# Optimization experiments

Hardware: AMD Instinct MI355X
Metric: run time of the kernel (lower is better)

Reference implementation:

```python
import jax, jax.numpy as jnp
import numpy as np

B, C, D, H, W = 2, 64, 12, 256, 64


def _conv1x1_relu(x, w, b):
    # x: (B, C, D, H, W); w: (C_out, C_in); b: (C_out,)
    y = jnp.einsum('oc,bcdhw->bodhw', w, x) + b[None, :, None, None, None]
    return jax.nn.relu(y)


def setup_inputs() -> dict:
    key = jax.random.key(0)
    ks = jax.random.split(key, 9)
    s = 1.0 / np.sqrt(C)
    inp = {
        'rep': jax.random.normal(ks[0], (B, C, D, H, W), dtype=jnp.float32),
        'Wq_w': jax.random.normal(ks[1], (C, C), dtype=jnp.float32) * s,
        'Wq_b': jnp.zeros((C,), dtype=jnp.float32),
        'Wk_w': jax.random.normal(ks[2], (C, C), dtype=jnp.float32) * s,
        'Wk_b': jnp.zeros((C,), dtype=jnp.float32),
        'Wv_w': jax.random.normal(ks[3], (C, C), dtype=jnp.float32) * s,
        'Wv_b': jnp.zeros((C,), dtype=jnp.float32),
        'FC_w': jax.random.normal(ks[4], (C, C), dtype=jnp.float32) * s,
        'FC_b': jnp.zeros((C,), dtype=jnp.float32),
    }
    return inp


def reference(rep, Wq_w, Wq_b, Wk_w, Wk_b, Wv_w, Wv_b, FC_w, FC_b):
    # 1x1x1 conv projections + ReLU, then permute to (B, D, W, H, C)
    q = _conv1x1_relu(rep, Wq_w, Wq_b).transpose(0, 2, 4, 3, 1)
    k = _conv1x1_relu(rep, Wk_w, Wk_b).transpose(0, 2, 4, 3, 1)
    v = _conv1x1_relu(rep, Wv_w, Wv_b).transpose(0, 2, 4, 3, 1)
    # attention over H axis: scores (B, D, W, H, H)
    scores = jnp.einsum('bdwhc,bdwgc->bdwhg', q, k) / jnp.sqrt(jnp.asarray(C, rep.dtype))
    attn = jax.nn.softmax(scores, axis=-1)
    out = jnp.einsum('bdwhg,bdwgc->bdwhc', attn, v)
    # permute(0,4,1,3,2): (B, D, W, H, C) -> (B, C, D, H, W)
    out = out.transpose(0, 4, 1, 3, 2)
    return _conv1x1_relu(out, FC_w, FC_b)
```

## Files before the change

### kernel.cpp

```cpp
#include <hip/hip_runtime.h>

typedef float f32x4 __attribute__((ext_vector_type(4)));
typedef short bf16x8 __attribute__((ext_vector_type(8)));
typedef unsigned short ushort_t;

#define NB 2
#define NC 64
#define ND 12
#define NH 256
#define NW 64
#define CSTRIDE (ND*NH*NW)
#define QSZ_ELEMS (24*64*256*64)
#define WS_NEED   ((size_t)3*QSZ_ELEMS*2)

__device__ __forceinline__ ushort_t bf_round(float f){
    unsigned int u = __float_as_uint(f);
    return (ushort_t)((u + 0x7fffu + ((u >> 16) & 1u)) >> 16);
}
__device__ __forceinline__ float bf_to_f(ushort_t s){ return __uint_as_float(((unsigned int)s) << 16); }

union U4S8 { uint4 u; bf16x8 s; };

__device__ __forceinline__ int row64_off(int r, int o){
    return r*128 + ((((o>>3) ^ (r&7)))<<4) + (o&7)*2;
}
__device__ __forceinline__ int row64_chunk(int r, int kchunk){
    return r*128 + (((kchunk ^ (r&7)))<<4);
}
__device__ __forceinline__ int vt_off(int c, int g){
    return c*512 + ((((g>>3) ^ (c&7)))<<4) + (g&7)*2;
}
__device__ __forceinline__ int vt_chunk(int c, int gchunk){
    return c*512 + (((gchunk ^ (c&7)))<<4);
}

__device__ __forceinline__ U4S8 wfrag_f(const float* W, int hl, int G, int ot, int m){
    const float* p2 = W + (hl + 16*ot)*NC + 32*m + 8*G;
    float4 f0 = *(const float4*)p2;
    float4 f1 = *(const float4*)(p2 + 4);
    U4S8 u; ushort_t* s = (ushort_t*)&u;
    s[0]=bf_round(f0.x); s[1]=bf_round(f0.y); s[2]=bf_round(f0.z); s[3]=bf_round(f0.w);
    s[4]=bf_round(f1.x); s[5]=bf_round(f1.y); s[6]=bf_round(f1.z); s[7]=bf_round(f1.w);
    return u;
}

__global__ __launch_bounds__(256, 2) void k1_proj(
    const float* __restrict__ rep,
    const float* __restrict__ Wq, const float* __restrict__ bq,
    const float* __restrict__ Wk, const float* __restrict__ bk,
    const float* __restrict__ Wv, const float* __restrict__ bv,
    ushort_t* __restrict__ qws, ushort_t* __restrict__ kws, ushort_t* __restrict__ vws)
{
    __shared__ __align__(16) unsigned char smem[65536];
    unsigned char* XL = smem;
    unsigned char* OB = smem + 32768;

    const int t = threadIdx.x, lane = t & 63, wid = t >> 6;
    const int G = lane >> 4, hl = lane & 15;
    const int blk = blockIdx.x;
    const int bd = blk >> 6;
    const int h0 = (blk & 63) * 4;
    const int d = bd % ND, b = bd / ND;
    const long dbase2 = (long)b*NC*CSTRIDE + (long)d*(NH*NW) + (long)h0*NW;

#pragma unroll
    for (int oct = 0; oct < 8; ++oct){
        float f[8];
#pragma unroll
        for (int j = 0; j < 8; ++j)
            f[j] = rep[dbase2 + (long)(8*oct + j)*CSTRIDE + t];
        U4S8 u; ushort_t* s = (ushort_t*)&u;
#pragma unroll
        for (int j = 0; j < 8; ++j) s[j] = bf_round(f[j]);
        *(uint4*)(XL + row64_chunk(t, oct)) = u.u;
    }
    __syncthreads();

    U4S8 xa[4][2];
#pragma unroll
    for (int nt = 0; nt < 4; ++nt)
#pragma unroll
        for (int m = 0; m < 2; ++m)
            xa[nt][m].u = *(const uint4*)(XL + row64_chunk(64*wid + 16*nt + hl, 4*m + G));

    auto pass = [&](const float* W, const float* bias, float scale, ushort_t* dst){
        U4S8 bw[4][2];
        float bb[4];
#pragma unroll
        for (int ot = 0; ot < 4; ++ot){
            bw[ot][0] = wfrag_f(W, hl, G, ot, 0);
            bw[ot][1] = wfrag_f(W, hl, G, ot, 1);
            bb[ot] = bias[hl + 16*ot];
        }
        f32x4 acc[4][4];
#pragma unroll
        for (int nt = 0; nt < 4; ++nt)
#pragma unroll
            for (int ot = 0; ot < 4; ++ot){
                f32x4 a = {0.f,0.f,0.f,0.f};
                a = __builtin_amdgcn_mfma_f32_16x16x32_bf16(xa[nt][0].s, bw[ot][0].s, a, 0,0,0);
                a = __builtin_amdgcn_mfma_f32_16x16x32_bf16(xa[nt][1].s, bw[ot][1].s, a, 0,0,0);
#pragma unroll
                for (int r = 0; r < 4; ++r) a[r] = fmaxf(a[r] + bb[ot], 0.f) * scale;
                acc[nt][ot] = a;
            }
#pragma unroll
        for (int nt = 0; nt < 4; ++nt)
#pragma unroll
            for (int ot = 0; ot < 4; ++ot)
#pragma unroll
                for (int r = 0; r < 4; ++r){
                    int n = 64*wid + 16*nt + 4*G + r;
                    int o = hl + 16*ot;
                    *(ushort_t*)(OB + row64_off(n, o)) = bf_round(acc[nt][ot][r]);
                }
        __syncthreads();
#pragma unroll
        for (int i = 0; i < 8; ++i){
            int g2 = i*256 + t; int n = g2 >> 3; int c8 = g2 & 7;
            uint4 u = *(const uint4*)(OB + row64_chunk(n, c8));
            long row_g = ((long)bd*64 + (n & 63))*256 + h0 + (n >> 6);
            *(uint4*)((unsigned char*)dst + row_g*128 + c8*16) = u;
        }
        __syncthreads();
    };
    pass(Wq, bq, 0.125f, qws);
    pass(Wk, bk, 1.0f,   kws);
    pass(Wv, bv, 1.0f,   vws);
}

__global__ __launch_bounds__(256, 2) void k2_attn(
    ushort_t* __restrict__ qws, const ushort_t* __restrict__ kws, const ushort_t* __restrict__ vws)
{
    __shared__ __align__(16) unsigned char smem[65536];
    unsigned char* KL = smem;
    unsigned char* VT = smem + 32768;

    const int t = threadIdx.x, lane = t & 63, wid = t >> 6;
    const int G = lane >> 4, hl = lane & 15;
    const int bdw = blockIdx.x;
    ushort_t* qslice = qws + (size_t)bdw*16384;
    const unsigned char* kslice = (const unsigned char*)(kws + (size_t)bdw*16384);
    const unsigned char* vslice = (const unsigned char*)(vws + (size_t)bdw*16384);

#pragma unroll
    for (int i = 0; i < 8; ++i){
        int g2 = i*256 + t; int g = g2 >> 3; int c8 = g2 & 7;
        uint4 ku = *(const uint4*)(kslice + g2*16);
        *(uint4*)(KL + row64_chunk(g, c8)) = ku;
        U4S8 vu; vu.u = *(const uint4*)(vslice + g2*16);
#pragma unroll
        for (int j = 0; j < 8; ++j)
            *(ushort_t*)(VT + vt_off(8*c8 + j, g)) = (ushort_t)vu.s[j];
    }
    __syncthreads();

    U4S8 qfr[4][2];
#pragma unroll
    for (int ht = 0; ht < 4; ++ht)
#pragma unroll
        for (int m = 0; m < 2; ++m)
            qfr[ht][m].u = *(const uint4*)((const unsigned char*)qslice
                              + (64*wid + 16*ht + hl)*128 + (4*m + G)*16);

    f32x4 oacc[4][4];
#pragma unroll
    for (int ct = 0; ct < 4; ++ct)
#pragma unroll
        for (int ht = 0; ht < 4; ++ht) oacc[ct][ht] = (f32x4){0.f,0.f,0.f,0.f};
    float m_run[4], l_run[4];
#pragma unroll
    for (int ht = 0; ht < 4; ++ht){ m_run[ht] = -1e30f; l_run[ht] = 0.f; }

    const int srcq0 = (16*((2*G    ) & 3) + hl)*4;
    const int srcq1 = (16*((2*G + 1) & 3) + hl)*4;

    for (int gb = 0; gb < NH; gb += 64){
        U4S8 kfr[4][2];
#pragma unroll
        for (int gt = 0; gt < 4; ++gt)
#pragma unroll
            for (int m = 0; m < 2; ++m)
                kfr[gt][m].u = *(const uint4*)(KL + row64_chunk(gb + 16*gt + hl, 4*m + G));

        f32x4 sacc[4][4];
#pragma unroll
        for (int gt = 0; gt < 4; ++gt)
#pragma unroll
            for (int ht = 0; ht < 4; ++ht){
                f32x4 a = {0.f,0.f,0.f,0.f};
                a = __builtin_amdgcn_mfma_f32_16x16x32_bf16(kfr[gt][0].s, qfr[ht][0].s, a, 0,0,0);
                a = __builtin_amdgcn_mfma_f32_16x16x32_bf16(kfr[gt][1].s, qfr[ht][1].s, a, 0,0,0);
                sacc[gt][ht] = a;
            }

        unsigned int pk[4][4][2];
#pragma unroll
        for (int ht = 0; ht < 4; ++ht){
            float cm = -1e30f;
#pragma unroll
            for (int gt = 0; gt < 4; ++gt)
#pragma unroll
                for (int r = 0; r < 4; ++r) cm = fmaxf(cm, sacc[gt][ht][r]);
            cm = fmaxf(cm, __shfl_xor(cm, 16));
            cm = fmaxf(cm, __shfl_xor(cm, 32));
            const float mn  = fmaxf(m_run[ht], cm);
            const float corr = __expf(m_run[ht] - mn);
            m_run[ht] = mn;
            float ls = 0.f;
#pragma unroll
            for (int gt = 0; gt < 4; ++gt){
                f32x4 s = sacc[gt][ht];
                float e0 = __expf(s[0]-mn), e1 = __expf(s[1]-mn);
                float e2 = __expf(s[2]-mn), e3 = __expf(s[3]-mn);
                ls += (e0+e1)+(e2+e3);
                pk[ht][gt][0] = (unsigned int)bf_round(e0) | ((unsigned int)bf_round(e1) << 16);
                pk[ht][gt][1] = (unsigned int)bf_round(e2) | ((unsigned int)bf_round(e3) << 16);
            }
            ls += __shfl_xor(ls, 16);
            ls += __shfl_xor(ls, 32);
            l_run[ht] = l_run[ht]*corr + ls;
#pragma unroll
            for (int ct = 0; ct < 4; ++ct)
#pragma unroll
                for (int r = 0; r < 4; ++r) oacc[ct][ht][r] *= corr;
        }

        U4S8 vfr[4][2];
#pragma unroll
        for (int ct = 0; ct < 4; ++ct)
#pragma unroll
            for (int m = 0; m < 2; ++m)
                vfr[ct][m].u = *(const uint4*)(VT + vt_chunk(16*ct + hl, (gb>>3) + 4*m + G));

#pragma unroll
        for (int m = 0; m < 2; ++m){
            U4S8 bfr[4];
#pragma unroll
            for (int ht = 0; ht < 4; ++ht){
                unsigned int wv[4];
#pragma unroll
                for (int jj = 0; jj < 4; ++jj){
                    const int src = (jj >> 1) ? srcq1 : srcq0;
                    const int p2  = jj & 1;
                    int rA = __builtin_amdgcn_ds_bpermute(src, (int)pk[ht][2*m  ][p2]);
                    int rB = __builtin_amdgcn_ds_bpermute(src, (int)pk[ht][2*m+1][p2]);
                    wv[jj] = (lane < 32) ? (unsigned int)rA : (unsigned int)rB;
                }
                bfr[ht].u = make_uint4(wv[0], wv[1], wv[2], wv[3]);
            }
#pragma unroll
            for (int ct = 0; ct < 4; ++ct)
#pragma unroll
                for (int ht = 0; ht < 4; ++ht)
                    oacc[ct][ht] = __builtin_amdgcn_mfma_f32_16x16x32_bf16(vfr[ct][m].s, bfr[ht].s, oacc[ct][ht], 0,0,0);
        }
    }

    float invl[4];
#pragma unroll
    for (int ht = 0; ht < 4; ++ht) invl[ht] = 1.f / l_run[ht];

    __syncthreads();
#pragma unroll
    for (int ct = 0; ct < 4; ++ct)
#pragma unroll
        for (int ht = 0; ht < 4; ++ht)
#pragma unroll
            for (int r = 0; r < 4; ++r){
                int h = 64*wid + 16*ht + hl;
                int c = 16*ct + 4*G + r;
                *(ushort_t*)(KL + row64_off(h, c)) = bf_round(oacc[ct][ht][r] * invl[ht]);
            }
    __syncthreads();
#pragma unroll
    for (int i = 0; i < 8; ++i){
        int g2 = i*256 + t;
        uint4 u = *(const uint4*)(KL + row64_chunk(g2 >> 3, g2 & 7));
        *(uint4*)((unsigned char*)qslice + g2*16) = u;
    }
}

__global__ __launch_bounds__(256, 2) void k3_fc(
    const ushort_t* __restrict__ ows, const float* __restrict__ Wf, const float* __restrict__ bfc,
    float* __restrict__ out)
{
    __shared__ __align__(16) float YL[16384];

    const int t = threadIdx.x, lane = t & 63, wid = t >> 6;
    const int G = lane >> 4, hl = lane & 15;
    const int blk = blockIdx.x;
    const int bd = blk >> 6;
    const int h0 = (blk & 63) * 4;
    const int d = bd % ND, b = bd / ND;

    U4S8 xa[4][2];
#pragma unroll
    for (int nt = 0; nt < 4; ++nt)
#pragma unroll
        for (int m = 0; m < 2; ++m){
            long row_g = ((long)bd*64 + (16*nt + hl))*256 + h0 + wid;
            xa[nt][m].u = *(const uint4*)((const unsigned char*)ows + row_g*128 + (4*m + G)*16);
        }

    U4S8 bw[4][2];
    float bb[4];
#pragma unroll
    for (int ot = 0; ot < 4; ++ot){
        bw[ot][0] = wfrag_f(Wf, hl, G, ot, 0);
        bw[ot][1] = wfrag_f(Wf, hl, G, ot, 1);
        bb[ot] = bfc[hl + 16*ot];
    }

    f32x4 acc[4][4];
#pragma unroll
    for (int nt = 0; nt < 4; ++nt)
#pragma unroll
        for (int ot = 0; ot < 4; ++ot){
            f32x4 a = {0.f,0.f,0.f,0.f};
            a = __builtin_amdgcn_mfma_f32_16x16x32_bf16(xa[nt][0].s, bw[ot][0].s, a, 0,0,0);
            a = __builtin_amdgcn_mfma_f32_16x16x32_bf16(xa[nt][1].s, bw[ot][1].s, a, 0,0,0);
#pragma unroll
            for (int r = 0; r < 4; ++r) a[r] = fmaxf(a[r] + bb[ot], 0.f);
            acc[nt][ot] = a;
        }

#pragma unroll
    for (int nt = 0; nt < 4; ++nt)
#pragma unroll
        for (int ot = 0; ot < 4; ++ot)
#pragma unroll
            for (int r = 0; r < 4; ++r){
                int n = 64*wid + 16*nt + 4*G + r;
                int o = hl + 16*ot;
                YL[(n<<6) + (o ^ ((n>>2)&31))] = acc[nt][ot][r];
            }
    __syncthreads();

    const long base3 = (long)b*NC*CSTRIDE + (long)d*(NH*NW) + (long)h0*NW;
#pragma unroll
    for (int i = 0; i < 16; ++i){
        int idx = i*1024 + t*4;
        int o = idx >> 8;
        int n0 = idx & 255;
        int osw = o ^ (t & 31);
        float4 v;
        v.x = YL[((n0+0)<<6) + osw];
        v.y = YL[((n0+1)<<6) + osw];
        v.z = YL[((n0+2)<<6) + osw];
        v.w = YL[((n0+3)<<6) + osw];
        *(float4*)(&out[base3 + (long)o*CSTRIDE + n0]) = v;
    }
}

__global__ __launch_bounds__(256, 2) void sa_mfma(
    const float* __restrict__ rep,
    const float* __restrict__ Wq, const float* __restrict__ bq,
    const float* __restrict__ Wk, const float* __restrict__ bk,
    const float* __restrict__ Wv, const float* __restrict__ bv,
    const float* __restrict__ Wf, const float* __restrict__ bfc,
    float* __restrict__ out)
{
    __shared__ __align__(16) unsigned char smem[65536];
    unsigned char* BUFA = smem;
    unsigned char* BUFB = smem + 32768;

    const int t = threadIdx.x, lane = t & 63, wid = t >> 6;
    const int G = lane >> 4, hl = lane & 15;
    const int j = blockIdx.x;
    const int x = j & 7;
    const int p = j >> 3;
    const int group = ((p >> 6) << 3) + x;
    const int w = p & 63;
    const int d = group % ND;
    const int b = group / ND;
    const long base_bd = (long)b*(NC*CSTRIDE) + (long)d*(NH*NW) + w;

    {
        const int h = t;
        const long rbase = base_bd + (long)h*NW;
#pragma unroll
        for (int c8 = 0; c8 < 8; ++c8){
            U4S8 u;
            ushort_t* s = (ushort_t*)&u;
#pragma unroll
            for (int jj = 0; jj < 8; ++jj)
                s[jj] = bf_round(rep[rbase + (long)(c8*8 + jj)*CSTRIDE]);
            *(uint4*)(BUFB + row64_chunk(h, c8)) = u.u;
        }
    }
    U4S8 xafr[4][2];
#pragma unroll
    for (int ht = 0; ht < 4; ++ht)
#pragma unroll
        for (int m = 0; m < 2; ++m)
            xafr[ht][m].u = *(const uint4*)(BUFB + row64_chunk(64*wid + 16*ht + hl, 4*m + G));

    auto do_proj = [&](const float* W, const float* bias, float scale, f32x4 (&acc)[4][4]){
        U4S8 bw[4][2];
#pragma unroll
        for (int ot = 0; ot < 4; ++ot){ bw[ot][0] = wfrag_f(W, hl, G, ot, 0); bw[ot][1] = wfrag_f(W, hl, G, ot, 1); }
        float bb[4];
#pragma unroll
        for (int ot = 0; ot < 4; ++ot) bb[ot] = bias[hl + 16*ot];
#pragma unroll
        for (int ht = 0; ht < 4; ++ht)
#pragma unroll
            for (int ot = 0; ot < 4; ++ot){
                f32x4 a = {0.f, 0.f, 0.f, 0.f};
                a = __builtin_amdgcn_mfma_f32_16x16x32_bf16(xafr[ht][0].s, bw[ot][0].s, a, 0, 0, 0);
                a = __builtin_amdgcn_mfma_f32_16x16x32_bf16(xafr[ht][1].s, bw[ot][1].s, a, 0, 0, 0);
#pragma unroll
                for (int r = 0; r < 4; ++r) a[r] = fmaxf(a[r] + bb[ot], 0.f) * scale;
                acc[ht][ot] = a;
            }
    };

    {
        f32x4 qa[4][4];
        do_proj(Wq, bq, 0.125f, qa);
#pragma unroll
        for (int ht = 0; ht < 4; ++ht)
#pragma unroll
            for (int ot = 0; ot < 4; ++ot)
#pragma unroll
                for (int r = 0; r < 4; ++r){
                    int h = 64*wid + 16*ht + 4*G + r;
                    int o = hl + 16*ot;
                    *(ushort_t*)(BUFA + row64_off(h, o)) = bf_round(qa[ht][ot][r]);
                }
    }
    U4S8 qfr[4][2];
#pragma unroll
    for (int ht = 0; ht < 4; ++ht)
#pragma unroll
        for (int m = 0; m < 2; ++m)
            qfr[ht][m].u = *(const uint4*)(BUFA + row64_chunk(64*wid + 16*ht + hl, 4*m + G));

    {
        f32x4 ka[4][4];
        do_proj(Wk, bk, 1.0f, ka);
#pragma unroll
        for (int gt = 0; gt < 4; ++gt)
#pragma unroll
            for (int ot = 0; ot < 4; ++ot)
#pragma unroll
                for (int r = 0; r < 4; ++r){
                    int g = 64*wid + 16*gt + 4*G + r;
                    int o = hl + 16*ot;
                    *(ushort_t*)(BUFA + row64_off(g, o)) = bf_round(ka[gt][ot][r]);
                }
    }
    f32x4 va[4][4];
    do_proj(Wv, bv, 1.0f, va);
    __syncthreads();
#pragma unroll
    for (int gt = 0; gt < 4; ++gt)
#pragma unroll
        for (int ot = 0; ot < 4; ++ot)
#pragma unroll
            for (int r = 0; r < 4; ++r){
                int g = 64*wid + 16*gt + 4*G + r;
                int c = hl + 16*ot;
                *(ushort_t*)(BUFB + vt_off(c, g)) = bf_round(va[gt][ot][r]);
            }
    __syncthreads();

    f32x4 oacc[4][4];
#pragma unroll
    for (int ct = 0; ct < 4; ++ct)
#pragma unroll
        for (int ht = 0; ht < 4; ++ht) oacc[ct][ht] = (f32x4){0.f,0.f,0.f,0.f};
    float m_run[4], l_run[4];
#pragma unroll
    for (int ht = 0; ht < 4; ++ht){ m_run[ht] = -1e30f; l_run[ht] = 0.f; }

    const int srcq0 = (16*((2*G    ) & 3) + hl)*4;
    const int srcq1 = (16*((2*G + 1) & 3) + hl)*4;

    for (int gb = 0; gb < NH; gb += 64){
        U4S8 kfr[4][2];
#pragma unroll
        for (int gt = 0; gt < 4; ++gt)
#pragma unroll
            for (int m = 0; m < 2; ++m)
                kfr[gt][m].u = *(const uint4*)(BUFA + row64_chunk(gb + 16*gt + hl, 4*m + G));

        f32x4 sacc[4][4];
#pragma unroll
        for (int gt = 0; gt < 4; ++gt)
#pragma unroll
            for (int ht = 0; ht < 4; ++ht){
                f32x4 a = {0.f,0.f,0.f,0.f};
                a = __builtin_amdgcn_mfma_f32_16x16x32_bf16(kfr[gt][0].s, qfr[ht][0].s, a, 0,0,0);
                a = __builtin_amdgcn_mfma_f32_16x16x32_bf16(kfr[gt][1].s, qfr[ht][1].s, a, 0,0,0);
                sacc[gt][ht] = a;
            }

        unsigned int pk[4][4][2];
#pragma unroll
        for (int ht = 0; ht < 4; ++ht){
            float cm = -1e30f;
#pragma unroll
            for (int gt = 0; gt < 4; ++gt)
#pragma unroll
                for (int r = 0; r < 4; ++r) cm = fmaxf(cm, sacc[gt][ht][r]);
            cm = fmaxf(cm, __shfl_xor(cm, 16));
            cm = fmaxf(cm, __shfl_xor(cm, 32));
            const float mn  = fmaxf(m_run[ht], cm);
            const float corr = __expf(m_run[ht] - mn);
            m_run[ht] = mn;
            float ls = 0.f;
#pragma unroll
            for (int gt = 0; gt < 4; ++gt){
                f32x4 s = sacc[gt][ht];
                float e0 = __expf(s[0]-mn), e1 = __expf(s[1]-mn);
                float e2 = __expf(s[2]-mn), e3 = __expf(s[3]-mn);
                ls += (e0+e1)+(e2+e3);
                pk[ht][gt][0] = (unsigned int)bf_round(e0) | ((unsigned int)bf_round(e1) << 16);
                pk[ht][gt][1] = (unsigned int)bf_round(e2) | ((unsigned int)bf_round(e3) << 16);
            }
            ls += __shfl_xor(ls, 16);
            ls += __shfl_xor(ls, 32);
            l_run[ht] = l_run[ht]*corr + ls;
#pragma unroll
            for (int ct = 0; ct < 4; ++ct)
#pragma unroll
                for (int r = 0; r < 4; ++r) oacc[ct][ht][r] *= corr;
        }

        U4S8 vfr[4][2];
#pragma unroll
        for (int ct = 0; ct < 4; ++ct)
#pragma unroll
            for (int m = 0; m < 2; ++m)
                vfr[ct][m].u = *(const uint4*)(BUFB + vt_chunk(16*ct + hl, (gb>>3) + 4*m + G));

#pragma unroll
        for (int m = 0; m < 2; ++m){
            U4S8 bfr[4];
#pragma unroll
            for (int ht = 0; ht < 4; ++ht){
                unsigned int wv[4];
#pragma unroll
                for (int jj = 0; jj < 4; ++jj){
                    const int src = (jj >> 1) ? srcq1 : srcq0;
                    const int p2  = jj & 1;
                    int rA = __builtin_amdgcn_ds_bpermute(src, (int)pk[ht][2*m  ][p2]);
                    int rB = __builtin_amdgcn_ds_bpermute(src, (int)pk[ht][2*m+1][p2]);
                    wv[jj] = (lane < 32) ? (unsigned int)rA : (unsigned int)rB;
                }
                bfr[ht].u = make_uint4(wv[0], wv[1], wv[2], wv[3]);
            }
#pragma unroll
            for (int ct = 0; ct < 4; ++ct)
#pragma unroll
                for (int ht = 0; ht < 4; ++ht)
                    oacc[ct][ht] = __builtin_amdgcn_mfma_f32_16x16x32_bf16(vfr[ct][m].s, bfr[ht].s, oacc[ct][ht], 0,0,0);
        }
    }

    float invl[4];
#pragma unroll
    for (int ht = 0; ht < 4; ++ht) invl[ht] = 1.f / l_run[ht];
    __syncthreads();
#pragma unroll
    for (int ct = 0; ct < 4; ++ct)
#pragma unroll
        for (int ht = 0; ht < 4; ++ht)
#pragma unroll
            for (int r = 0; r < 4; ++r){
                float v = oacc[ct][ht][r] * invl[ht];
                ushort_t hi = bf_round(v);
                ushort_t lo = bf_round(v - bf_to_f(hi));
                int hrow = 64*wid + 16*ht + hl;
                int c = 16*ct + 4*G + r;
                *(ushort_t*)(BUFA + row64_off(hrow, c)) = hi;
                *(ushort_t*)(BUFB + row64_off(hrow, c)) = lo;
            }
    U4S8 bh[4][2], bl[4][2];
#pragma unroll
    for (int ht = 0; ht < 4; ++ht)
#pragma unroll
        for (int m = 0; m < 2; ++m){
            bh[ht][m].u = *(const uint4*)(BUFA + row64_chunk(64*wid + 16*ht + hl, 4*m + G));
            bl[ht][m].u = *(const uint4*)(BUFB + row64_chunk(64*wid + 16*ht + hl, 4*m + G));
        }

    f32x4 yacc[4][4];
#pragma unroll
    for (int ot = 0; ot < 4; ++ot)
#pragma unroll
        for (int ht = 0; ht < 4; ++ht) yacc[ot][ht] = (f32x4){0.f,0.f,0.f,0.f};
#pragma unroll
    for (int ot = 0; ot < 4; ++ot)
#pragma unroll
        for (int m = 0; m < 2; ++m){
            U4S8 wf = wfrag_f(Wf, hl, G, ot, m);
#pragma unroll
            for (int ht = 0; ht < 4; ++ht){
                yacc[ot][ht] = __builtin_amdgcn_mfma_f32_16x16x32_bf16(wf.s, bh[ht][m].s, yacc[ot][ht], 0,0,0);
                yacc[ot][ht] = __builtin_amdgcn_mfma_f32_16x16x32_bf16(wf.s, bl[ht][m].s, yacc[ot][ht], 0,0,0);
            }
        }
    float bfv[4][4];
#pragma unroll
    for (int ot = 0; ot < 4; ++ot)
#pragma unroll
        for (int r = 0; r < 4; ++r) bfv[ot][r] = bfc[16*ot + 4*G + r];
#pragma unroll
    for (int ot = 0; ot < 4; ++ot)
#pragma unroll
        for (int ht = 0; ht < 4; ++ht)
#pragma unroll
            for (int r = 0; r < 4; ++r){
                int o = 16*ot + 4*G + r;
                int h = 64*wid + 16*ht + hl;
                float y = fmaxf(yacc[ot][ht][r] + bfv[ot][r], 0.f);
                out[base_bd + (long)o*CSTRIDE + (long)h*NW] = y;
            }
}

extern "C" void kernel_launch(void* const* d_in, const int* in_sizes, int n_in,
                              void* d_out, int out_size, void* d_ws, size_t ws_size,
                              hipStream_t stream) {
    (void)in_sizes; (void)n_in; (void)out_size;
    const float* rep = (const float*)d_in[0];
    const float* Wq  = (const float*)d_in[1];
    const float* bq  = (const float*)d_in[2];
    const float* Wk  = (const float*)d_in[3];
    const float* bk  = (const float*)d_in[4];
    const float* Wv  = (const float*)d_in[5];
    const float* bv  = (const float*)d_in[6];
    const float* Wf  = (const float*)d_in[7];
    const float* bfc = (const float*)d_in[8];
    float* out = (float*)d_out;

    if (ws_size >= WS_NEED) {
        ushort_t* qws = (ushort_t*)d_ws;
        ushort_t* kws = qws + QSZ_ELEMS;
        ushort_t* vws = kws + QSZ_ELEMS;
        k1_proj<<<dim3(1536), dim3(256), 0, stream>>>(rep, Wq, bq, Wk, bk, Wv, bv, qws, kws, vws);
        k2_attn<<<dim3(1536), dim3(256), 0, stream>>>(qws, kws, vws);
        k3_fc  <<<dim3(1536), dim3(256), 0, stream>>>(qws, Wf, bfc, out);
    } else {
        sa_mfma<<<dim3(1536), dim3(256), 0, stream>>>(rep, Wq, bq, Wk, bk, Wv, bv, Wf, bfc, out);
    }
}
```

Before: 172.4 us.

## Make projection kernel LDS-free with one wave per block

The projection kernel now launches single-wave blocks with four times as many blocks. Each wave loads its input fragments straight from global memory into MFMA registers and writes the bf16 results directly to the workspace. This removes the shared-memory staging and the transpose buffers, along with their barriers, and frees LDS so more blocks can be resident. The trade-off is that the output stores become scattered 2-byte writes instead of coalesced 16-byte rows, and the input loads are less coalesced.

Result: slower. 222.5 us (+29.1%).

```diff
diff --git a/kernel.cpp b/kernel.cpp
--- a/kernel.cpp
+++ b/kernel.cpp
@@ -44,57 +44,53 @@
     return u;
 }
 
-__global__ __launch_bounds__(256, 2) void k1_proj(
+__global__ __launch_bounds__(64, 4) void k1_proj(
     const float* __restrict__ rep,
     const float* __restrict__ Wq, const float* __restrict__ bq,
     const float* __restrict__ Wk, const float* __restrict__ bk,
     const float* __restrict__ Wv, const float* __restrict__ bv,
     ushort_t* __restrict__ qws, ushort_t* __restrict__ kws, ushort_t* __restrict__ vws)
 {
-    __shared__ __align__(16) unsigned char smem[65536];
-    unsigned char* XL = smem;
-    unsigned char* OB = smem + 32768;
-
-    const int t = threadIdx.x, lane = t & 63, wid = t >> 6;
+    const int lane = threadIdx.x & 63;
     const int G = lane >> 4, hl = lane & 15;
     const int blk = blockIdx.x;
-    const int bd = blk >> 6;
-    const int h0 = (blk & 63) * 4;
+    const int wid   = blk & 3;
+    const int h0idx = (blk >> 2) & 63;
+    const int bd    = blk >> 8;
     const int d = bd % ND, b = bd / ND;
-    const long dbase2 = (long)b*NC*CSTRIDE + (long)d*(NH*NW) + (long)h0*NW;
-
-#pragma unroll
-    for (int oct = 0; oct < 8; ++oct){
-        float f[8];
-#pragma unroll
-        for (int j = 0; j < 8; ++j)
-            f[j] = rep[dbase2 + (long)(8*oct + j)*CSTRIDE + t];
-        U4S8 u; ushort_t* s = (ushort_t*)&u;
-#pragma unroll
-        for (int j = 0; j < 8; ++j) s[j] = bf_round(f[j]);
-        *(uint4*)(XL + row64_chunk(t, oct)) = u.u;
-    }
-    __syncthreads();
+    const int h = h0idx*4 + wid;
+    const long xbase = (long)b*NC*CSTRIDE + (long)d*(NH*NW) + (long)h*NW;
 
     U4S8 xa[4][2];
 #pragma unroll
-    for (int nt = 0; nt < 4; ++nt)
+    for (int nt = 0; nt < 4; ++nt){
+        float f[16];
 #pragma unroll
         for (int m = 0; m < 2; ++m)
-            xa[nt][m].u = *(const uint4*)(XL + row64_chunk(64*wid + 16*nt + hl, 4*m + G));
+#pragma unroll
+            for (int j = 0; j < 8; ++j)
+                f[m*8+j] = rep[xbase + (long)(32*m + 8*G + j)*CSTRIDE + 16*nt + hl];
+#pragma unroll
+        for (int m = 0; m < 2; ++m){
+            ushort_t* s = (ushort_t*)&xa[nt][m];
+#pragma unroll
+            for (int j = 0; j < 8; ++j) s[j] = bf_round(f[m*8+j]);
+        }
+    }
+
+    const long wsbase = (long)bd*64*256;
 
     auto pass = [&](const float* W, const float* bias, float scale, ushort_t* dst){
-        U4S8 bw[4][2];
-        float bb[4];
+        U4S8 bw[4][2]; float bb[4];
 #pragma unroll
         for (int ot = 0; ot < 4; ++ot){
             bw[ot][0] = wfrag_f(W, hl, G, ot, 0);
             bw[ot][1] = wfrag_f(W, hl, G, ot, 1);
             bb[ot] = bias[hl + 16*ot];
         }
-        f32x4 acc[4][4];
-#pragma unroll
-        for (int nt = 0; nt < 4; ++nt)
+#pragma unroll
+        for (int nt = 0; nt < 4; ++nt){
+            f32x4 acc[4];
 #pragma unroll
             for (int ot = 0; ot < 4; ++ot){
                 f32x4 a = {0.f,0.f,0.f,0.f};
@@ -102,27 +98,16 @@
                 a = __builtin_amdgcn_mfma_f32_16x16x32_bf16(xa[nt][1].s, bw[ot][1].s, a, 0,0,0);
 #pragma unroll
                 for (int r = 0; r < 4; ++r) a[r] = fmaxf(a[r] + bb[ot], 0.f) * scale;
-                acc[nt][ot] = a;
-            }
-#pragma unroll
-        for (int nt = 0; nt < 4; ++nt)
-#pragma unroll
-            for (int ot = 0; ot < 4; ++ot)
-#pragma unroll
-                for (int r = 0; r < 4; ++r){
-                    int n = 64*wid + 16*nt + 4*G + r;
-                    int o = hl + 16*ot;
-                    *(ushort_t*)(OB + row64_off(n, o)) = bf_round(acc[nt][ot][r]);
+                acc[ot] = a;
+            }
+#pragma unroll
+            for (int r = 0; r < 4; ++r)
+#pragma unroll
+                for (int ot = 0; ot < 4; ++ot){
+                    long row = wsbase + (long)(16*nt + 4*G + r)*256 + h;
+                    dst[row*64 + hl + 16*ot] = bf_round(acc[ot][r]);
                 }
-        __syncthreads();
-#pragma unroll
-        for (int i = 0; i < 8; ++i){
-            int g2 = i*256 + t; int n = g2 >> 3; int c8 = g2 & 7;
-            uint4 u = *(const uint4*)(OB + row64_chunk(n, c8));
-            long row_g = ((long)bd*64 + (n & 63))*256 + h0 + (n >> 6);
-            *(uint4*)((unsigned char*)dst + row_g*128 + c8*16) = u;
-        }
-        __syncthreads();
+        }
     };
     pass(Wq, bq, 0.125f, qws);
     pass(Wk, bk, 1.0f,   kws);
@@ -640,7 +625,7 @@
         ushort_t* qws = (ushort_t*)d_ws;
         ushort_t* kws = qws + QSZ_ELEMS;
         ushort_t* vws = kws + QSZ_ELEMS;
-        k1_proj<<<dim3(1536), dim3(256), 0, stream>>>(rep, Wq, bq, Wk, bk, Wv, bv, qws, kws, vws);
+        k1_proj<<<dim3(6144), dim3(64),  0, stream>>>(rep, Wq, bq, Wk, bk, Wv, bv, qws, kws, vws);
         k2_attn<<<dim3(1536), dim3(256), 0, stream>>>(qws, kws, vws);
         k3_fc  <<<dim3(1536), dim3(256), 0, stream>>>(qws, Wf, bfc, out);
     } else {
```
